# Performance work log

Measured on AMD Instinct MI355X. Metric: run time of the kernel, lower is better.

The kernel has to match this reference:

```python
import math
import jax, jax.numpy as jnp
import numpy as np

E = 1024
H = 16
DH = E // H
R = 8
ALPHA = 16
LORA_S = ALPHA / R

def build_slopes(h):
    start = 2 ** (-2 ** (-(math.log2(h) - 3)))
    return jnp.asarray([start * start ** i for i in range(h)], dtype=jnp.float32)

def setup_inputs() -> dict:
    key = jax.random.key(0)
    ks = jax.random.split(key, 12)
    B, T = 2, 2048
    x = jax.random.normal(ks[0], (B, T, E), dtype=jnp.float32)
    # nn.Linear weights: [out_f, in_f]; LoRA A: [out_f, r], B: [r, in_f]
    def lin(k):
        return jax.random.normal(k, (E, E), dtype=jnp.float32) / math.sqrt(E)
    inp = {
        "x": x,
        "Wq": lin(ks[1]), "Aq": jax.random.normal(ks[2], (E, R)) * 0.01, "Bq": jax.random.normal(ks[3], (R, E)) * 0.01,
        "Wk": lin(ks[4]), "Ak": jax.random.normal(ks[5], (E, R)) * 0.01, "Bk": jax.random.normal(ks[6], (R, E)) * 0.01,
        "Wv": lin(ks[7]), "Av": jax.random.normal(ks[8], (E, R)) * 0.01, "Bv": jax.random.normal(ks[9], (R, E)) * 0.01,
        "Wp": lin(ks[10]),
    }
    return inp

def _lora(x, W, A, Bm):
    # x @ W.T + (x @ B.T) @ A.T * s
    return x @ W.T + ((x @ Bm.T) @ A.T) * LORA_S

def reference(x, Wq, Aq, Bq, Wk, Ak, Bk, Wv, Av, Bv, Wp):
    B, T, _ = x.shape
    slopes = build_slopes(H)  # [H]
    q = _lora(x, Wq, Aq, Bq).reshape(B, T, H, DH).transpose(0, 2, 1, 3)  # [B,H,T,dh]
    k = _lora(x, Wk, Ak, Bk).reshape(B, T, H, DH).transpose(0, 2, 1, 3)
    v = _lora(x, Wv, Av, Bv).reshape(B, T, H, DH).transpose(0, 2, 1, 3)
    s = jnp.einsum("bhqd,bhkd->bhqk", q, k) / math.sqrt(DH)
    i = jnp.arange(T, dtype=jnp.float32)[:, None]
    j = jnp.arange(T, dtype=jnp.float32)[None, :]
    alibi = slopes[:, None, None] * (i - j)  # [H,T,T]
    mask = jnp.triu(jnp.full((T, T), -jnp.inf, dtype=jnp.float32), 1)
    s = s + alibi[None] + mask
    p = jax.nn.softmax(s, axis=-1)
    o = jnp.einsum("bhqk,bhkd->bhqd", p, v).transpose(0, 2, 1, 3).reshape(B, T, E)
    return o @ Wp.T
```

## Files before the change

kernel.cpp:

```cpp
#include <hip/hip_runtime.h>

typedef unsigned short u16;
typedef unsigned int   u32;
typedef __bf16 bf16_t;
typedef bf16_t bf16x8 __attribute__((ext_vector_type(8)));
typedef bf16_t bf16x2v __attribute__((ext_vector_type(2)));
typedef float  f32x4  __attribute__((ext_vector_type(4)));

#define E_DIM 1024
#define T_DIM 2048
#define H_NUM 16
#define DH 64
#define BT 4096
#define Y_LD 2048

__device__ __forceinline__ u16 f2bf(float f) {
  u32 u = __builtin_bit_cast(u32, f);
  u32 r = (u + 0x7fffu + ((u >> 16) & 1u)) >> 16;
  return (u16)r;
}

__device__ __forceinline__ float fexp2(float x) {
#if __has_builtin(__builtin_amdgcn_exp2f)
  return __builtin_amdgcn_exp2f(x);
#else
  return exp2f(x);
#endif
}

__device__ __forceinline__ int swz(int r, int c) {
  return r * 64 + (c ^ ((r & 7) << 3));
}

__device__ __forceinline__ void store_val(float* p, float v) { *p = v; }
__device__ __forceinline__ void store_val(u16* p, float v)   { *p = f2bf(v); }

typedef __attribute__((address_space(3))) unsigned int as3_u32;
typedef const __attribute__((address_space(1))) unsigned int as1_u32;

__device__ __forceinline__ void async16(const u16* g, u16* l) {
  __builtin_amdgcn_global_load_lds((as1_u32*)g, (as3_u32*)l, 16, 0, 0);
}

__device__ __forceinline__ u32 pack2(float a, float b) {
  bf16x2v v;
  v[0] = (bf16_t)a;
  v[1] = (bf16_t)b;
  return __builtin_bit_cast(u32, v);
}

__device__ __forceinline__ void plswap(u32& a, u32& b) {
#if __has_builtin(__builtin_amdgcn_permlane32_swap)
  typedef u32 u32x2 __attribute__((ext_vector_type(2)));
  u32x2 r = __builtin_amdgcn_permlane32_swap(a, b, false, false);
  a = r[0];
  b = r[1];
#else
  asm volatile("v_permlane32_swap_b32 %0, %1" : "+v"(a), "+v"(b));
#endif
}

__device__ __forceinline__ void redist_pair(u32 A, u32 B, bool odd, u32& wj, u32& wj2) {
  plswap(A, B);
  u32 sA = __builtin_amdgcn_ds_swizzle(A, 0x401F);
  u32 sB = __builtin_amdgcn_ds_swizzle(B, 0x401F);
  wj  = odd ? sB : A;
  wj2 = odd ? B : sA;
}

__global__ __launch_bounds__(256) void k_prep(
    const float* __restrict__ x,
    const float* __restrict__ W0, const float* __restrict__ A0, const float* __restrict__ B0,
    const float* __restrict__ W1, const float* __restrict__ A1, const float* __restrict__ B1,
    const float* __restrict__ W2, const float* __restrict__ A2, const float* __restrict__ B2,
    const float* __restrict__ Wp,
    u16* __restrict__ xb, u16* __restrict__ Weff, u16* __restrict__ Wpb, float s0) {
  const int blk = blockIdx.x;
  const int tid = threadIdx.x;
  if (blk < 4096) {
    int i = (blk * 256 + tid) * 4;
    float4 v = *reinterpret_cast<const float4*>(x + i);
    u32 lo = (u32)f2bf(v.x) | ((u32)f2bf(v.y) << 16);
    u32 hi = (u32)f2bf(v.z) | ((u32)f2bf(v.w) << 16);
    *reinterpret_cast<uint2*>(xb + i) = make_uint2(lo, hi);
  } else if (blk < 7168) {
    int e4 = (blk - 4096) * 256 + tid;
    int m = e4 >> 18;
    int e = (e4 & 262143) * 4;
    const float* W  = (m == 0) ? W0 : (m == 1) ? W1 : W2;
    const float* A  = (m == 0) ? A0 : (m == 1) ? A1 : A2;
    const float* Bm = (m == 0) ? B0 : (m == 1) ? B1 : B2;
    const float sc  = (m == 0) ? s0 : 1.0f;
    int o = e >> 10, i = e & 1023;
    float4 wv = *reinterpret_cast<const float4*>(W + e);
    float acc[4] = {wv.x, wv.y, wv.z, wv.w};
#pragma unroll
    for (int r = 0; r < 8; ++r) {
      float a2 = 2.0f * A[o * 8 + r];
      float4 bv = *reinterpret_cast<const float4*>(Bm + r * 1024 + i);
      acc[0] += a2 * bv.x; acc[1] += a2 * bv.y; acc[2] += a2 * bv.z; acc[3] += a2 * bv.w;
    }
    u32 lo = (u32)f2bf(acc[0] * sc) | ((u32)f2bf(acc[1] * sc) << 16);
    u32 hi = (u32)f2bf(acc[2] * sc) | ((u32)f2bf(acc[3] * sc) << 16);
    *reinterpret_cast<uint2*>(Weff + (size_t)m * 1048576 + e) = make_uint2(lo, hi);
  } else {
    int i = ((blk - 7168) * 256 + tid) * 4;
    float4 v = *reinterpret_cast<const float4*>(Wp + i);
    u32 lo = (u32)f2bf(v.x) | ((u32)f2bf(v.y) << 16);
    u32 hi = (u32)f2bf(v.z) | ((u32)f2bf(v.w) << 16);
    *reinterpret_cast<uint2*>(Wpb + i) = make_uint2(lo, hi);
  }
}

template <typename OUT_T, bool QKV>
__global__ __launch_bounds__(256) void k_gemm_bt(
    const u16* __restrict__ A, const u16* __restrict__ B,
    OUT_T* __restrict__ C, u16* __restrict__ Vt, int K, int ldc) {
  __shared__ __align__(16) u16 As[128 * 64];
  __shared__ __align__(16) u16 Bs[128 * 64];
  const int tid  = threadIdx.x;
  const int lane = tid & 63;
  const int wave = tid >> 6;
  const int wr = wave >> 1, wc = wave & 1;
  const int m0 = blockIdx.y * 128;
  const int n0 = blockIdx.x * 128;
  const int lr = lane & 15;
  const int lk = (lane >> 4) * 8;
  const bool vmode = QKV && (n0 >= 2048);

  f32x4 acc[4][4] = {};

  for (int k0 = 0; k0 < K; k0 += 64) {
    __syncthreads();
#pragma unroll
    for (int p = 0; p < 4; ++p) {
      const int off = (p * 4 + wave) * 512;
      const int e = off + lane * 8;
      const int r = e >> 6, c = e & 63;
      const int cs = c ^ ((r & 7) << 3);
      async16(&A[(size_t)(m0 + r) * K + k0 + cs], As + off);
      async16(&B[(size_t)(n0 + r) * K + k0 + cs], Bs + off);
    }
    __syncthreads();
#pragma unroll
    for (int kk = 0; kk < 2; ++kk) {
      bf16x8 af[4], bfr[4];
#pragma unroll
      for (int mi = 0; mi < 4; ++mi)
        af[mi] = *reinterpret_cast<const bf16x8*>(&As[swz(wr * 64 + mi * 16 + lr, kk * 32 + lk)]);
#pragma unroll
      for (int ni = 0; ni < 4; ++ni)
        bfr[ni] = *reinterpret_cast<const bf16x8*>(&Bs[swz(wc * 64 + ni * 16 + lr, kk * 32 + lk)]);
      if (vmode) {
#pragma unroll
        for (int mi = 0; mi < 4; ++mi)
#pragma unroll
          for (int ni = 0; ni < 4; ++ni)
            acc[mi][ni] = __builtin_amdgcn_mfma_f32_16x16x32_bf16(bfr[ni], af[mi], acc[mi][ni], 0, 0, 0);
      } else {
#pragma unroll
        for (int mi = 0; mi < 4; ++mi)
#pragma unroll
          for (int ni = 0; ni < 4; ++ni)
            acc[mi][ni] = __builtin_amdgcn_mfma_f32_16x16x32_bf16(af[mi], bfr[ni], acc[mi][ni], 0, 0, 0);
      }
    }
  }
  const int rg = (lane >> 4) * 4;
  if (vmode) {
#pragma unroll
    for (int mi = 0; mi < 4; ++mi)
#pragma unroll
      for (int ni = 0; ni < 4; ++ni)
#pragma unroll
        for (int q = 0; q < 4; ++q) {
          int o = n0 - 2048 + wc * 64 + ni * 16 + rg + q;
          int h = o >> 6, d = o & 63;
          int rowm = m0 + wr * 64 + mi * 16 + lr;
          int b = rowm >> 11, t = rowm & 2047;
          Vt[(size_t)(((b << 4) + h) * 64 + d) * 2048 + t] = f2bf(acc[mi][ni][q]);
        }
  } else {
#pragma unroll
    for (int mi = 0; mi < 4; ++mi)
#pragma unroll
      for (int ni = 0; ni < 4; ++ni)
#pragma unroll
        for (int q = 0; q < 4; ++q) {
          int row = m0 + wr * 64 + mi * 16 + rg + q;
          int col = n0 + wc * 64 + ni * 16 + lr;
          store_val(&C[(size_t)row * ldc + col], acc[mi][ni][q]);
        }
  }
}

__global__ __launch_bounds__(256) void k_attn6(
    const u16* __restrict__ Y, const u16* __restrict__ Vt, u16* __restrict__ Og) {
  __shared__ __align__(16) u16 Ks[2][4096];
  __shared__ __align__(16) u16 Vs[2][4096];

  const int tid = threadIdx.x;
  const int lane = tid & 63;
  const int wave = tid >> 6;
  const int lr = lane & 15;
  const int lg = lane >> 4;
  const int lk = lg * 8;
  const bool odd = (lane & 16) != 0;

  const int orig = blockIdx.x;
  const int bh = orig & 31;
  const int hi = orig >> 5;
  const int j = hi >> 3, hh = hi & 7;
  const int qt = 31 - (j * 8 + ((j & 1) ? (7 - hh) : hh));
  const int b = bh >> 4, h = bh & 15;

  const float LOG2E = 1.4426950408889634f;
  const float slope2 = exp2f(-0.5f * (float)(h + 1)) * LOG2E;

  const u16* Kb = Y + (size_t)b * T_DIM * Y_LD + 1024 + h * DH;
  const u16* Vb = Vt + (size_t)bh * DH * T_DIM;

  bf16x8 qf[2];
  {
    const int qrow = qt * 64 + wave * 16 + lr;
#pragma unroll
    for (int kk = 0; kk < 2; ++kk)
      qf[kk] = *reinterpret_cast<const bf16x8*>(
          &Y[(size_t)(b * T_DIM + qrow) * Y_LD + h * DH + kk * 32 + lk]);
  }

  float nkb[16];
#pragma unroll
  for (int ni = 0; ni < 4; ++ni)
#pragma unroll
    for (int r = 0; r < 4; ++r)
      nkb[ni * 4 + r] = -slope2 * (float)(ni * 16 + lg * 4 + r) - 12.0f;

  bf16x8 ones;
#pragma unroll
  for (int jj = 0; jj < 8; ++jj) ones[jj] = (bf16_t)1.0f;

  f32x4 oacc[4] = {};
  f32x4 lacc = {};

  auto stage = [&](int bufi, int kt) {
    const int kv0 = kt * 64;
#pragma unroll
    for (int q = 0; q < 2; ++q) {
      const int off = (q * 4 + wave) * 512;
      const int e = off + lane * 8;
      const int r = e >> 6, c = e & 63;
      const int cs = c ^ ((r & 7) << 3);
      async16(Kb + (size_t)(kv0 + r) * Y_LD + cs, &Ks[bufi][off]);
      async16(Vb + (size_t)r * T_DIM + kv0 + cs, &Vs[bufi][off]);
    }
  };

  stage(0, 0);
  __syncthreads();
  int buf = 0;

  auto step = [&](int kt, bool DIAG, bool PREF) {
    if (PREF) stage(buf ^ 1, kt + 1);
    f32x4 s[4] = {};
#pragma unroll
    for (int kk = 0; kk < 2; ++kk)
#pragma unroll
      for (int ni = 0; ni < 4; ++ni) {
        bf16x8 kf = *reinterpret_cast<const bf16x8*>(&Ks[buf][swz(ni * 16 + lr, kk * 32 + lk)]);
        s[ni] = __builtin_amdgcn_mfma_f32_16x16x32_bf16(kf, qf[kk], s[ni], 0, 0, 0);
      }
    const float ck = -slope2 * (float)(kt * 64);
    u32 pk[4][2];
#pragma unroll
    for (int ni = 0; ni < 4; ++ni) {
      float p[4];
#pragma unroll
      for (int r = 0; r < 4; ++r) {
        float sc = s[ni][r] + nkb[ni * 4 + r] + ck;
        if (DIAG && (ni * 16 + lg * 4 + r) > (wave * 16 + lr)) sc = -INFINITY;
        p[r] = fexp2(sc);
      }
      pk[ni][0] = pack2(p[0], p[1]);
      pk[ni][1] = pack2(p[2], p[3]);
    }
    uint4 PW[2];
#pragma unroll
    for (int kk = 0; kk < 2; ++kk) {
      redist_pair(pk[2 * kk][0], pk[2 * kk + 1][0], odd, PW[kk].x, PW[kk].z);
      redist_pair(pk[2 * kk][1], pk[2 * kk + 1][1], odd, PW[kk].y, PW[kk].w);
    }
#pragma unroll
    for (int kk = 0; kk < 2; ++kk) {
      bf16x8 ph = __builtin_bit_cast(bf16x8, PW[kk]);
      lacc = __builtin_amdgcn_mfma_f32_16x16x32_bf16(ph, ones, lacc, 0, 0, 0);
#pragma unroll
      for (int f = 0; f < 4; ++f) {
        bf16x8 vf = *reinterpret_cast<const bf16x8*>(&Vs[buf][swz(f * 16 + lr, kk * 32 + lk)]);
        oacc[f] = __builtin_amdgcn_mfma_f32_16x16x32_bf16(ph, vf, oacc[f], 0, 0, 0);
      }
    }
    __syncthreads();
    buf ^= 1;
  };

  for (int kt = 0; kt < qt; ++kt) step(kt, false, true);
  step(qt, true, false);

  float linv[4];
#pragma unroll
  for (int r = 0; r < 4; ++r) linv[r] = 1.0f / lacc[r];
#pragma unroll
  for (int f = 0; f < 4; ++f)
#pragma unroll
    for (int r = 0; r < 4; ++r) {
      int q = qt * 64 + wave * 16 + lg * 4 + r;
      Og[(size_t)(b * T_DIM + q) * E_DIM + h * DH + f * 16 + lr] =
          f2bf(oacc[f][r] * linv[r]);
    }
}

extern "C" void kernel_launch(void* const* d_in, const int* in_sizes, int n_in,
                              void* d_out, int out_size, void* d_ws, size_t ws_size,
                              hipStream_t stream) {
  const float* x  = (const float*)d_in[0];
  const float* Wq = (const float*)d_in[1];
  const float* Aq = (const float*)d_in[2];
  const float* Bq = (const float*)d_in[3];
  const float* Wk = (const float*)d_in[4];
  const float* Ak = (const float*)d_in[5];
  const float* Bk = (const float*)d_in[6];
  const float* Wv = (const float*)d_in[7];
  const float* Av = (const float*)d_in[8];
  const float* Bv = (const float*)d_in[9];
  const float* Wp = (const float*)d_in[10];
  float* out = (float*)d_out;

  char* ws = (char*)d_ws;
  u16* xb   = (u16*)(ws);
  u16* Og   = (u16*)(ws);
  u16* Weff = (u16*)(ws + 8388608);
  u16* Wpb  = (u16*)(ws + 14680064);
  u16* Yq   = (u16*)(ws + 16777216);
  u16* VtB  = (u16*)(ws + 33554432);

  const float ISQ2 = 0.125f * 1.4426950408889634f;

  k_prep<<<8192, 256, 0, stream>>>(x, Wq, Aq, Bq, Wk, Ak, Bk, Wv, Av, Bv, Wp,
                                   xb, Weff, Wpb, ISQ2);
  {
    dim3 grid(24, 32);
    k_gemm_bt<u16, true><<<grid, 256, 0, stream>>>(xb, Weff, Yq, VtB, E_DIM, Y_LD);
  }
  k_attn6<<<1024, 256, 0, stream>>>(Yq, VtB, Og);
  {
    dim3 grid(8, 32);
    k_gemm_bt<float, false><<<grid, 256, 0, stream>>>(Og, Wpb, out, nullptr, E_DIM, E_DIM);
  }
}
```

Measured before the change: 117.2 us.

## Triple-buffer attention K/V tiles with vmcnt-based waits and MFMA priority hints

Changes the attention kernel from double to triple buffering of the K and V LDS tiles, prefetching two tiles ahead. Full __syncthreads is replaced by an explicit s_waitcnt vmcnt(4) plus s_barrier, so only the oldest tile's async loads must land before the barrier. s_setprio raises wave priority around the MFMA sections to favour matrix work. LDS use grows by half, which may reduce occupancy, and the hand-written vmcnt counting depends on each thread issuing exactly four loads per stage.

```diff
diff --git a/kernel.cpp b/kernel.cpp
--- a/kernel.cpp
+++ b/kernel.cpp
@@ -40,6 +40,14 @@
 
 __device__ __forceinline__ void async16(const u16* g, u16* l) {
   __builtin_amdgcn_global_load_lds((as1_u32*)g, (as3_u32*)l, 16, 0, 0);
+}
+
+template <int N>
+__device__ __forceinline__ void waitvm_barrier() {
+  if constexpr (N == 4) asm volatile("s_waitcnt vmcnt(4)" ::: "memory");
+  else                  asm volatile("s_waitcnt vmcnt(0)" ::: "memory");
+  __builtin_amdgcn_s_barrier();
+  __builtin_amdgcn_sched_barrier(0);
 }
 
 __device__ __forceinline__ u32 pack2(float a, float b) {
@@ -194,10 +202,10 @@
   }
 }
 
-__global__ __launch_bounds__(256) void k_attn6(
+__global__ __launch_bounds__(256) void k_attn7(
     const u16* __restrict__ Y, const u16* __restrict__ Vt, u16* __restrict__ Og) {
-  __shared__ __align__(16) u16 Ks[2][4096];
-  __shared__ __align__(16) u16 Vs[2][4096];
+  __shared__ __align__(16) u16 Ks[3][4096];
+  __shared__ __align__(16) u16 Vs[3][4096];
 
   const int tid = threadIdx.x;
   const int lane = tid & 63;
@@ -256,13 +264,9 @@
     }
   };
 
-  stage(0, 0);
-  __syncthreads();
-  int buf = 0;
-
-  auto step = [&](int kt, bool DIAG, bool PREF) {
-    if (PREF) stage(buf ^ 1, kt + 1);
+  auto step = [&](int kt, int buf, bool DIAG) {
     f32x4 s[4] = {};
+    __builtin_amdgcn_s_setprio(1);
 #pragma unroll
     for (int kk = 0; kk < 2; ++kk)
 #pragma unroll
@@ -270,6 +274,7 @@
         bf16x8 kf = *reinterpret_cast<const bf16x8*>(&Ks[buf][swz(ni * 16 + lr, kk * 32 + lk)]);
         s[ni] = __builtin_amdgcn_mfma_f32_16x16x32_bf16(kf, qf[kk], s[ni], 0, 0, 0);
       }
+    __builtin_amdgcn_s_setprio(0);
     const float ck = -slope2 * (float)(kt * 64);
     u32 pk[4][2];
 #pragma unroll
@@ -290,6 +295,7 @@
       redist_pair(pk[2 * kk][0], pk[2 * kk + 1][0], odd, PW[kk].x, PW[kk].z);
       redist_pair(pk[2 * kk][1], pk[2 * kk + 1][1], odd, PW[kk].y, PW[kk].w);
     }
+    __builtin_amdgcn_s_setprio(1);
 #pragma unroll
     for (int kk = 0; kk < 2; ++kk) {
       bf16x8 ph = __builtin_bit_cast(bf16x8, PW[kk]);
@@ -300,12 +306,27 @@
         oacc[f] = __builtin_amdgcn_mfma_f32_16x16x32_bf16(ph, vf, oacc[f], 0, 0, 0);
       }
     }
-    __syncthreads();
-    buf ^= 1;
+    __builtin_amdgcn_s_setprio(0);
   };
 
-  for (int kt = 0; kt < qt; ++kt) step(kt, false, true);
-  step(qt, true, false);
+  stage(0, 0);
+  if (qt >= 1) {
+    stage(1, 1);
+    waitvm_barrier<4>();
+  } else {
+    waitvm_barrier<0>();
+  }
+
+  int b0 = 0, b1 = 1, b2 = 2;
+  for (int kt = 0; kt < qt; ++kt) {
+    const bool pf = (kt + 2 <= qt);
+    if (pf) stage(b2, kt + 2);
+    step(kt, b0, false);
+    if (pf) waitvm_barrier<4>();
+    else    waitvm_barrier<0>();
+    int t = b0; b0 = b1; b1 = b2; b2 = t;
+  }
+  step(qt, b0, true);
 
   float linv[4];
 #pragma unroll
@@ -352,7 +373,7 @@
     dim3 grid(24, 32);
     k_gemm_bt<u16, true><<<grid, 256, 0, stream>>>(xb, Weff, Yq, VtB, E_DIM, Y_LD);
   }
-  k_attn6<<<1024, 256, 0, stream>>>(Yq, VtB, Og);
+  k_attn7<<<1024, 256, 0, stream>>>(Yq, VtB, Og);
   {
     dim3 grid(8, 32);
     k_gemm_bt<float, false><<<grid, 256, 0, stream>>>(Og, Wpb, out, nullptr, E_DIM, E_DIM);
```

Result: faster. 112.6 us (-3.9%).

## Split long causal attention query tiles across KV halves and merge partials

Applied to the files above, without the earlier changes.

Query tiles 16-31 are now processed by two blocks each: one covers KV tiles 0-15 and the other covers 16 through the diagonal. Each writes an unnormalized bf16 partial output and its row sums, and a new merge kernel adds the two and normalizes. Query tiles 0-15 still run as single blocks. The aim is to balance per-block work on the causal triangle and raise the block count from 1024 to 1536 to reduce tail imbalance. In exchange it adds an extra kernel launch, extra global traffic, and bf16 rounding of the partial sums. It also replaces __syncthreads with an explicit vmcnt wait plus barrier and adds s_setprio around the MFMA sections.

```diff
diff --git a/kernel.cpp b/kernel.cpp
--- a/kernel.cpp
+++ b/kernel.cpp
@@ -19,6 +19,10 @@
   u32 r = (u + 0x7fffu + ((u >> 16) & 1u)) >> 16;
   return (u16)r;
 }
+__device__ __forceinline__ float bf2f(u16 v) {
+  u32 u = ((u32)v) << 16;
+  return __builtin_bit_cast(float, u);
+}
 
 __device__ __forceinline__ float fexp2(float x) {
 #if __has_builtin(__builtin_amdgcn_exp2f)
@@ -40,6 +44,12 @@
 
 __device__ __forceinline__ void async16(const u16* g, u16* l) {
   __builtin_amdgcn_global_load_lds((as1_u32*)g, (as3_u32*)l, 16, 0, 0);
+}
+
+__device__ __forceinline__ void waitvm0_barrier() {
+  asm volatile("s_waitcnt vmcnt(0)" ::: "memory");
+  __builtin_amdgcn_s_barrier();
+  __builtin_amdgcn_sched_barrier(0);
 }
 
 __device__ __forceinline__ u32 pack2(float a, float b) {
@@ -194,8 +204,10 @@
   }
 }
 
-__global__ __launch_bounds__(256) void k_attn6(
-    const u16* __restrict__ Y, const u16* __restrict__ Vt, u16* __restrict__ Og) {
+__global__ __launch_bounds__(256) void k_attn8(
+    const u16* __restrict__ Y, const u16* __restrict__ Vt, u16* __restrict__ Og,
+    u16* __restrict__ Oa, u16* __restrict__ Ob,
+    float* __restrict__ la, float* __restrict__ lb) {
   __shared__ __align__(16) u16 Ks[2][4096];
   __shared__ __align__(16) u16 Vs[2][4096];
 
@@ -209,9 +221,10 @@
 
   const int orig = blockIdx.x;
   const int bh = orig & 31;
-  const int hi = orig >> 5;
-  const int j = hi >> 3, hh = hi & 7;
-  const int qt = 31 - (j * 8 + ((j & 1) ? (7 - hh) : hh));
+  const int c  = orig >> 5;
+  const int qt = (c < 16) ? (16 + c) : (47 - c);
+  const int ks = (c >= 16 && c < 32) ? 16 : 0;
+  const int ke = (c < 16) ? 15 : qt;
   const int b = bh >> 4, h = bh & 15;
 
   const float LOG2E = 1.4426950408889634f;
@@ -249,20 +262,16 @@
     for (int q = 0; q < 2; ++q) {
       const int off = (q * 4 + wave) * 512;
       const int e = off + lane * 8;
-      const int r = e >> 6, c = e & 63;
-      const int cs = c ^ ((r & 7) << 3);
+      const int r = e >> 6, cc = e & 63;
+      const int cs = cc ^ ((r & 7) << 3);
       async16(Kb + (size_t)(kv0 + r) * Y_LD + cs, &Ks[bufi][off]);
       async16(Vb + (size_t)r * T_DIM + kv0 + cs, &Vs[bufi][off]);
     }
   };
 
-  stage(0, 0);
-  __syncthreads();
-  int buf = 0;
-
-  auto step = [&](int kt, bool DIAG, bool PREF) {
-    if (PREF) stage(buf ^ 1, kt + 1);
+  auto step = [&](int kt, int buf, bool DIAG) {
     f32x4 s[4] = {};
+    __builtin_amdgcn_s_setprio(1);
 #pragma unroll
     for (int kk = 0; kk < 2; ++kk)
 #pragma unroll
@@ -270,6 +279,7 @@
         bf16x8 kf = *reinterpret_cast<const bf16x8*>(&Ks[buf][swz(ni * 16 + lr, kk * 32 + lk)]);
         s[ni] = __builtin_amdgcn_mfma_f32_16x16x32_bf16(kf, qf[kk], s[ni], 0, 0, 0);
       }
+    __builtin_amdgcn_s_setprio(0);
     const float ck = -slope2 * (float)(kt * 64);
     u32 pk[4][2];
 #pragma unroll
@@ -290,6 +300,7 @@
       redist_pair(pk[2 * kk][0], pk[2 * kk + 1][0], odd, PW[kk].x, PW[kk].z);
       redist_pair(pk[2 * kk][1], pk[2 * kk + 1][1], odd, PW[kk].y, PW[kk].w);
     }
+    __builtin_amdgcn_s_setprio(1);
 #pragma unroll
     for (int kk = 0; kk < 2; ++kk) {
       bf16x8 ph = __builtin_bit_cast(bf16x8, PW[kk]);
@@ -300,24 +311,74 @@
         oacc[f] = __builtin_amdgcn_mfma_f32_16x16x32_bf16(ph, vf, oacc[f], 0, 0, 0);
       }
     }
-    __syncthreads();
+    __builtin_amdgcn_s_setprio(0);
+  };
+
+  stage(0, ks);
+  waitvm0_barrier();
+  int buf = 0;
+  for (int kt = ks; kt <= ke; ++kt) {
+    if (kt < ke) stage(buf ^ 1, kt + 1);
+    step(kt, buf, kt == qt);
+    waitvm0_barrier();
     buf ^= 1;
-  };
-
-  for (int kt = 0; kt < qt; ++kt) step(kt, false, true);
-  step(qt, true, false);
-
-  float linv[4];
-#pragma unroll
-  for (int r = 0; r < 4; ++r) linv[r] = 1.0f / lacc[r];
-#pragma unroll
-  for (int f = 0; f < 4; ++f)
-#pragma unroll
-    for (int r = 0; r < 4; ++r) {
-      int q = qt * 64 + wave * 16 + lg * 4 + r;
-      Og[(size_t)(b * T_DIM + q) * E_DIM + h * DH + f * 16 + lr] =
-          f2bf(oacc[f][r] * linv[r]);
-    }
+  }
+
+  if (c >= 32) {
+    float linv[4];
+#pragma unroll
+    for (int r = 0; r < 4; ++r) linv[r] = 1.0f / lacc[r];
+#pragma unroll
+    for (int f = 0; f < 4; ++f)
+#pragma unroll
+      for (int r = 0; r < 4; ++r) {
+        int q = qt * 64 + wave * 16 + lg * 4 + r;
+        Og[(size_t)(b * T_DIM + q) * E_DIM + h * DH + f * 16 + lr] =
+            f2bf(oacc[f][r] * linv[r]);
+      }
+  } else {
+    u16* Op   = (c < 16) ? Oa : Ob;
+    float* lp = (c < 16) ? la : lb;
+#pragma unroll
+    for (int f = 0; f < 4; ++f)
+#pragma unroll
+      for (int r = 0; r < 4; ++r) {
+        int q = qt * 64 + wave * 16 + lg * 4 + r;
+        Op[(size_t)(b * 1024 + (q - 1024)) * E_DIM + h * DH + f * 16 + lr] =
+            f2bf(oacc[f][r]);
+      }
+    if (lr == 0) {
+#pragma unroll
+      for (int r = 0; r < 4; ++r) {
+        int q = qt * 64 + wave * 16 + lg * 4 + r;
+        lp[bh * 1024 + (q - 1024)] = lacc[r];
+      }
+    }
+  }
+}
+
+__global__ __launch_bounds__(256) void k_merge(
+    const u16* __restrict__ Oa, const u16* __restrict__ Ob,
+    const float* __restrict__ la, const float* __restrict__ lb,
+    u16* __restrict__ Og) {
+  int idx = blockIdx.x * 256 + threadIdx.x;
+  int row = idx >> 8;
+  int cg  = (idx & 255) * 4;
+  int b = row >> 10, tl = row & 1023;
+  int h = cg >> 6;
+  size_t po = (size_t)row * E_DIM + cg;
+  uint2 ua = *reinterpret_cast<const uint2*>(Oa + po);
+  uint2 ub = *reinterpret_cast<const uint2*>(Ob + po);
+  float l = la[((b << 4) + h) * 1024 + tl] + lb[((b << 4) + h) * 1024 + tl];
+  float inv = 1.0f / l;
+  const u16* pa = reinterpret_cast<const u16*>(&ua);
+  const u16* pb = reinterpret_cast<const u16*>(&ub);
+  u16 o[4];
+#pragma unroll
+  for (int j = 0; j < 4; ++j)
+    o[j] = f2bf((bf2f(pa[j]) + bf2f(pb[j])) * inv);
+  *reinterpret_cast<uint2*>(Og + (size_t)(b * T_DIM + 1024 + tl) * E_DIM + cg) =
+      *reinterpret_cast<const uint2*>(o);
 }
 
 extern "C" void kernel_launch(void* const* d_in, const int* in_sizes, int n_in,
@@ -337,12 +398,17 @@
   float* out = (float*)d_out;
 
   char* ws = (char*)d_ws;
+  const size_t MB = 1048576;
   u16* xb   = (u16*)(ws);
-  u16* Og   = (u16*)(ws);
-  u16* Weff = (u16*)(ws + 8388608);
-  u16* Wpb  = (u16*)(ws + 14680064);
-  u16* Yq   = (u16*)(ws + 16777216);
-  u16* VtB  = (u16*)(ws + 33554432);
+  u16* Oa   = (u16*)(ws);
+  u16* Ob   = (u16*)(ws + 4 * MB);
+  u16* Weff = (u16*)(ws + 8 * MB);
+  float* la = (float*)(ws + 8 * MB);
+  float* lb = (float*)(ws + 8 * MB + 131072);
+  u16* Yq   = (u16*)(ws + 14 * MB);
+  u16* VtB  = (u16*)(ws + 30 * MB);
+  u16* Wpb  = (u16*)(ws + 38 * MB);
+  u16* Og   = (u16*)(ws + 40 * MB);
 
   const float ISQ2 = 0.125f * 1.4426950408889634f;
 
@@ -352,7 +418,8 @@
     dim3 grid(24, 32);
     k_gemm_bt<u16, true><<<grid, 256, 0, stream>>>(xb, Weff, Yq, VtB, E_DIM, Y_LD);
   }
-  k_attn6<<<1024, 256, 0, stream>>>(Yq, VtB, Og);
+  k_attn8<<<1536, 256, 0, stream>>>(Yq, VtB, Og, Oa, Ob, la, lb);
+  k_merge<<<2048, 256, 0, stream>>>(Oa, Ob, la, lb, Og);
   {
     dim3 grid(8, 32);
     k_gemm_bt<float, false><<<grid, 256, 0, stream>>>(Og, Wpb, out, nullptr, E_DIM, E_DIM);
```

After: 112.7 us. 1.04x faster.
